# Optimization experiments

Measured on AMD Instinct MI355X. Metric: run time of the kernel, lower is better.

## Reference

```python
import jax, jax.numpy as jnp
import numpy as np

N_LINKS = 10000
N_PATHS = 100000
LSD = 32   # link_state_dim
PSD = 32   # path_state_dim
T = 4
MAX_LEN = 12
RU = 256   # readout_units
OUT = 2


def _glorot(key, shape):
    return jax.random.normal(key, shape) * jnp.sqrt(2.0 / (shape[0] + shape[-1]))


def setup_inputs() -> dict:
    key = jax.random.key(0)
    ks = jax.random.split(key, 12)
    # variable path lengths 4..12 (mean 8)
    lengths = 4 + (np.arange(N_PATHS) % 9)
    E = int(lengths.sum())
    offsets = np.cumsum(lengths) - lengths
    paths = np.repeat(np.arange(N_PATHS), lengths)
    seqs = np.arange(E) - np.repeat(offsets, lengths)  # position of hop within its path
    rng = np.random.default_rng(0)
    links = rng.integers(0, N_LINKS, size=E)
    return {
        "capacities": jax.random.uniform(ks[0], (N_LINKS,), minval=1.0, maxval=10.0),
        "traffic": jax.random.uniform(ks[1], (N_PATHS,), minval=0.1, maxval=1.0),
        "links": jnp.asarray(links, jnp.int32),
        "paths": jnp.asarray(paths, jnp.int32),
        "seqs": jnp.asarray(seqs, jnp.int32),
        "n_links": N_LINKS,
        "n_paths": N_PATHS,
        "K_link": _glorot(ks[2], (LSD, 3 * LSD)),
        "R_link": _glorot(ks[3], (LSD, 3 * LSD)),
        "b_link": jnp.zeros((2, 3 * LSD)),
        "K_path": _glorot(ks[4], (LSD, 3 * PSD)),
        "R_path": _glorot(ks[5], (PSD, 3 * PSD)),
        "b_path": jnp.zeros((2, 3 * PSD)),
        "W1": _glorot(ks[6], (PSD, RU)),
        "b1": jnp.zeros((RU,)),
        "W2": _glorot(ks[7], (RU, RU)),
        "b2": jnp.zeros((RU,)),
        "Wf": _glorot(ks[8], (RU + PSD, OUT)),
        "bf": jnp.zeros((OUT,)),
    }


def _gru(x, h, K, R, b):
    # keras GRUCell, reset_after=True: separate input/recurrent biases
    xz = x @ K + b[0]
    hz = h @ R + b[1]
    xi_z, xi_r, xi_h = jnp.split(xz, 3, axis=-1)
    hi_z, hi_r, hi_h = jnp.split(hz, 3, axis=-1)
    z = jax.nn.sigmoid(xi_z + hi_z)
    r = jax.nn.sigmoid(xi_r + hi_r)
    hh = jnp.tanh(xi_h + r * hi_h)
    return z * h + (1.0 - z) * hh


def reference(capacities, traffic, links, paths, seqs, n_links, n_paths,
              K_link, R_link, b_link, K_path, R_path, b_path,
              W1, b1, W2, b2, Wf, bf):
    link_state = jnp.concatenate([capacities[:, None], jnp.zeros((n_links, LSD - 1))], axis=1)
    path_state = jnp.concatenate([traffic[:, None], jnp.zeros((n_paths, PSD - 1))], axis=1)

    lens = jax.ops.segment_sum(jnp.ones_like(paths), paths, num_segments=n_paths)  # [P]
    mask_t = (jnp.arange(MAX_LEN)[:, None] < lens[None, :])  # [L, P]

    for _ in range(T):
        h_ = link_state[links]  # gather: [E, LSD]
        # scatter into padded per-path sequences: [P, L, LSD]
        padded = jnp.zeros((n_paths, MAX_LEN, LSD), link_state.dtype).at[paths, seqs].set(h_)

        def step(h, xm):
            x_t, m_t = xm  # [P, LSD], [P]
            h_new = _gru(x_t, h, K_path, R_path, b_path)
            h = jnp.where(m_t[:, None], h_new, h)  # masked steps keep state
            return h, h

        path_state, outputs = jax.lax.scan(step, path_state, (padded.transpose(1, 0, 2), mask_t))
        m = outputs[seqs, paths]  # gather_nd: [E, PSD]
        m = jax.ops.segment_sum(m, links, num_segments=n_links)  # [n_links, PSD]
        link_state = _gru(m, link_state, K_link, R_link, b_link)

    h1 = jax.nn.selu(path_state @ W1 + b1)
    h2 = jax.nn.selu(h1 @ W2 + b2)
    pred = jnp.concatenate([h2, path_state], axis=1) @ Wf + bf
    return pred
```

## Files before the change

kernel.cpp:

```cpp
#include <hip/hip_runtime.h>
#include <hip/hip_bf16.h>

#define NPATHS 100000
#define NLINKS 10000
#define TITERS 4
#define GRP    695

typedef __hip_bfloat16 bf16;
typedef unsigned short u16;
typedef unsigned int   u32;
typedef _Float16 half8 __attribute__((ext_vector_type(8)));
typedef __attribute__((ext_vector_type(4))) float float4v;

#define U_LNK 64
#define U_KPB 320064
#define U_RPB 323136
#define U_KLB 326208
#define U_RLB 329280
#define U_W1T 332352
#define U_W2T 340544
#define F_BP  203040
#define F_BL  203232
#define F_B1  203424
#define F_B2  203680
#define F_WF  203936
#define F_MAC 204544
#define U_WFP 1049088
#define F_PS  524800

__device__ __forceinline__ float bf2f(bf16 v) { return __bfloat162float(v); }
__device__ __forceinline__ u16 f2h_u(float f) {
    _Float16 h = (_Float16)f; u16 u; __builtin_memcpy(&u, &h, 2); return u;
}
__device__ __forceinline__ float h2f_u(u16 u) {
    _Float16 h; __builtin_memcpy(&h, &u, 2); return (float)h;
}
__device__ __forceinline__ float loadf(const void* p, int i, int isbf) {
    return isbf ? bf2f(((const bf16*)p)[i]) : ((const float*)p)[i];
}
__device__ __forceinline__ float sigmoid_(float v) { return 1.f / (1.f + __expf(-v)); }
__device__ __forceinline__ float tanh_(float v) { return 1.f - 2.f / (__expf(2.f * v) + 1.f); }
__device__ __forceinline__ float selu_(float v) {
    return v > 0.f ? 1.0507009873554805f * v : 1.7580993408473766f * (__expf(v) - 1.f);
}
__device__ __forceinline__ u16* ps_row(u16* ps0, u16* ps1, u16* ps2, int p) {
    return p < 49999 ? ps0 + (size_t)p * 32
         : (p < 99998 ? ps1 + (size_t)(p - 49999) * 32
                      : ps2 + (size_t)(p - 99998) * 32);
}

__global__ void probe_kernel(const u32* __restrict__ cap, int* __restrict__ flag) {
    if (threadIdx.x == 0 && blockIdx.x == 0) {
        bool ok = true;
        for (int i = 0; i < 8; ++i) {
            u32 w = cap[i];
            u32 e1 = (w >> 7) & 0xFF, e2 = (w >> 23) & 0xFF;
            ok = ok && e1 >= 122 && e1 <= 133 && e2 >= 122 && e2 <= 133;
        }
        *flag = ok ? 1 : 0;
    }
}

__global__ __launch_bounds__(256) void init_kernel(
    const void* __restrict__ traf, const void* __restrict__ cap, const int* __restrict__ flag,
    float* __restrict__ wsf, u16* __restrict__ wsu, u16* ps0, u16* ps1, u16* ps2,
    const void* Kp, const void* Rp, const void* bp,
    const void* Kl, const void* Rl, const void* bl,
    const void* W1, const void* b1, const void* W2, const void* b2,
    const void* Wf, const void* bfv)
{
    const int isbf = *flag;
    const int i = blockIdx.x * 256 + threadIdx.x;
    if (i < NPATHS) {
        u32 ww[16];
        ww[0] = (u32)f2h_u(loadf(traf, i, isbf));
#pragma unroll
        for (int k = 1; k < 16; ++k) ww[k] = 0;
        uint4* row = (uint4*)ps_row(ps0, ps1, ps2, i);
        row[0] = *(uint4*)(ww + 0);  row[1] = *(uint4*)(ww + 4);
        row[2] = *(uint4*)(ww + 8);  row[3] = *(uint4*)(ww + 12);
    }
    int j;
    j = i;          if (j >= 0 && j < 320000)
        wsu[U_LNK + j] = ((j & 31) == 0) ? f2h_u(loadf(cap, j >> 5, isbf)) : (u16)0;
    j = i - 320000; if (j >= 0 && j < 3072) {
        int t = j >> 9, lane = (j >> 3) & 63, e = j & 7;
        int k = (lane >> 4) * 8 + e, n = t * 16 + (lane & 15);
        wsu[U_KPB + j] = f2h_u(loadf(Kp, k * 96 + n, isbf));
    }
    j = i - 323072; if (j >= 0 && j < 3072) {
        int t = j >> 9, lane = (j >> 3) & 63, e = j & 7;
        int k = (lane >> 4) * 8 + e, n = t * 16 + (lane & 15);
        wsu[U_RPB + j] = f2h_u(loadf(Rp, k * 96 + n, isbf));
    }
    j = i - 326144; if (j >= 0 && j < 3072) {
        int t = j >> 9, lane = (j >> 3) & 63, e = j & 7;
        int k = (lane >> 4) * 8 + e, n = t * 16 + (lane & 15);
        wsu[U_KLB + j] = f2h_u(loadf(Kl, k * 96 + n, isbf));
    }
    j = i - 329216; if (j >= 0 && j < 3072) {
        int t = j >> 9, lane = (j >> 3) & 63, e = j & 7;
        int k = (lane >> 4) * 8 + e, n = t * 16 + (lane & 15);
        wsu[U_RLB + j] = f2h_u(loadf(Rl, k * 96 + n, isbf));
    }
    j = i - 332288; if (j >= 0 && j < 192)   wsf[F_BP + j] = loadf(bp, j, isbf);
    j = i - 332480; if (j >= 0 && j < 192)   wsf[F_BL + j] = loadf(bl, j, isbf);
    j = i - 332672; if (j >= 0 && j < 256)   wsf[F_B1 + j] = loadf(b1, j, isbf);
    j = i - 332928; if (j >= 0 && j < 256)   wsf[F_B2 + j] = loadf(b2, j, isbf);
    j = i - 333184; if (j >= 0 && j < 578)
        wsf[F_WF + j] = (j < 576) ? loadf(Wf, j, isbf) : loadf(bfv, j - 576, isbf);
    j = i - 334000; if (j >= 0 && j < 8192) {
        int t = j >> 9, lane = (j >> 3) & 63, e = j & 7;
        int k = (lane >> 4) * 8 + e, n = t * 16 + (lane & 15);
        wsu[U_W1T + j] = f2h_u(loadf(W1, k * 256 + n, isbf));
    }
    j = i - 343000; if (j >= 0 && j < 65536) {
        int g = j >> 9, kb = g >> 4, t = g & 15;
        int lane = (j >> 3) & 63, e = j & 7;
        int k = kb * 32 + (lane >> 4) * 8 + e, n = t * 16 + (lane & 15);
        wsu[U_W2T + j] = f2h_u(loadf(W2, k * 256 + n, isbf));
    }
    j = i - 408576; if (j >= 0 && j < 512) {
        int lane = j >> 3, e = j & 7;
        int k = (lane >> 4) * 8 + e, n = lane & 15;
        wsu[U_WFP + j] = (n < 2) ? f2h_u(loadf(Wf, (256 + k) * 2 + n, isbf)) : (u16)0;
    }
}

__global__ __launch_bounds__(256, 3) void path_gru_mfma(
    const int* __restrict__ links,
    const u16* __restrict__ KPB, const u16* __restrict__ RPB,
    const float* __restrict__ bp,
    const u16* __restrict__ lnk16,
    u16* ps0, u16* ps1, u16* ps2, float* __restrict__ m_acc)
{
    __shared__ u16 hlds[4][16 * 40];
    const int tid = threadIdx.x;
    const int wv = tid >> 6, lane = tid & 63;
    const int q = lane >> 4, col = lane & 15;
    const int c = blockIdx.x % 9;
    const int gi = (blockIdx.x / 9) * 4 + wv;
    if (gi >= GRP) return;
    const int cnt = (c == 0) ? 11112 : 11111;
    const int idx0 = gi * 16;
    const int L = 4 + c;

    const int idxc = idx0 + col;
    const int actc = idxc < cnt;
    const int idcl = min(idxc, cnt - 1);
    const int pc   = c + 9 * idcl;
    const int offc = 4 * pc + idcl * 36 + (c * (c - 1)) / 2;

    u16* hw = hlds[wv];

    half8 KB[6], RB[6];
#pragma unroll
    for (int t = 0; t < 6; ++t) {
        KB[t] = *(const half8*)(KPB + t * 512 + lane * 8);
        RB[t] = *(const half8*)(RPB + t * 512 + lane * 8);
    }
    float xzb[6], hzb[6];
#pragma unroll
    for (int t = 0; t < 6; ++t) { xzb[t] = bp[t * 16 + col]; hzb[t] = bp[96 + t * 16 + col]; }

    half8 Ah = *(const half8*)(ps_row(ps0, ps1, ps2, pc) + q * 8);
    float hold[2][4];
#pragma unroll
    for (int t = 0; t < 2; ++t)
#pragma unroll
        for (int r = 0; r < 4; ++r) {
            int idr = min(idx0 + q * 4 + r, cnt - 1);
            int pr = c + 9 * idr;
            hold[t][r] = h2f_u(ps_row(ps0, ps1, ps2, pr)[t * 16 + col]);
        }

    int ln = actc ? links[offc] : -1;
    half8 Ax = *(const half8*)(lnk16 + (size_t)max(ln, 0) * 32 + q * 8);

    for (int s = 0; s < L; ++s) {
        const int ln_nxt = (s + 1 < L && actc) ? links[offc + s + 1] : -1;
        const half8 Ax_nxt = *(const half8*)(lnk16 + (size_t)max(ln_nxt, 0) * 32 + q * 8);

        float4v xz[6], hz[6];
#pragma unroll
        for (int t = 0; t < 6; ++t) {
            float4v ix = {xzb[t], xzb[t], xzb[t], xzb[t]};
            float4v ih = {hzb[t], hzb[t], hzb[t], hzb[t]};
            xz[t] = __builtin_amdgcn_mfma_f32_16x16x32_f16(Ax, KB[t], ix, 0, 0, 0);
            hz[t] = __builtin_amdgcn_mfma_f32_16x16x32_f16(Ah, RB[t], ih, 0, 0, 0);
        }
#pragma unroll
        for (int t = 0; t < 2; ++t)
#pragma unroll
            for (int r = 0; r < 4; ++r) {
                const float z  = sigmoid_(xz[t][r] + hz[t][r]);
                const float rr = sigmoid_(xz[t + 2][r] + hz[t + 2][r]);
                const float hh = tanh_(xz[t + 4][r] + rr * hz[t + 4][r]);
                const float hn = z * hold[t][r] + (1.f - z) * hh;
                hold[t][r] = hn;
                hw[(q * 4 + r) * 40 + t * 16 + col] = f2h_u(hn);
            }
        Ah = *(const half8*)(hw + col * 40 + q * 8);
        const int half_ = lane >> 5, kk = lane & 31;
#pragma unroll
        for (int j2 = 0; j2 < 8; ++j2) {
            const int src = 2 * j2 + half_;
            const int tgt = __shfl(ln, src);
            const float v = h2f_u(hw[src * 40 + kk]);
            if (tgt >= 0) unsafeAtomicAdd(m_acc + (size_t)tgt * 32 + kk, v);
        }
        ln = ln_nxt; Ax = Ax_nxt;
    }
    if (actc) {
        uint4 tmp; __builtin_memcpy(&tmp, &Ah, 16);
        *(uint4*)(ps_row(ps0, ps1, ps2, pc) + q * 8) = tmp;
    }
}

__global__ __launch_bounds__(256) void link_gru_mfma(
    const u16* __restrict__ KLB, const u16* __restrict__ RLB,
    const float* __restrict__ bl,
    float* __restrict__ m_io, u16* __restrict__ lnk16)
{
    __shared__ u16 hlds[4][16 * 40];
    const int tid = threadIdx.x;
    const int wv = tid >> 6, lane = tid & 63;
    const int q = lane >> 4, col = lane & 15;
    const int w = blockIdx.x * 4 + wv;
    if (w >= NLINKS / 16) return;
    const int base = w * 16;
    u16* hw = hlds[wv];

    half8 KB[6], RB[6];
#pragma unroll
    for (int t = 0; t < 6; ++t) {
        KB[t] = *(const half8*)(KLB + t * 512 + lane * 8);
        RB[t] = *(const half8*)(RLB + t * 512 + lane * 8);
    }
    float xzb[6], hzb[6];
#pragma unroll
    for (int t = 0; t < 6; ++t) { xzb[t] = bl[t * 16 + col]; hzb[t] = bl[96 + t * 16 + col]; }

    half8 Ax;
    {
        float4* mr = (float4*)(m_io + (size_t)(base + col) * 32 + q * 8);
        float4 a = mr[0], b = mr[1];
        _Float16 xv[8] = {(_Float16)a.x, (_Float16)a.y, (_Float16)a.z, (_Float16)a.w,
                          (_Float16)b.x, (_Float16)b.y, (_Float16)b.z, (_Float16)b.w};
        __builtin_memcpy(&Ax, xv, 16);
        const float4 z4 = make_float4(0.f, 0.f, 0.f, 0.f);
        mr[0] = z4; mr[1] = z4;
    }
    half8 Ah = *(const half8*)(lnk16 + (size_t)(base + col) * 32 + q * 8);
    float hold[2][4];
#pragma unroll
    for (int t = 0; t < 2; ++t)
#pragma unroll
        for (int r = 0; r < 4; ++r)
            hold[t][r] = h2f_u(lnk16[(size_t)(base + q * 4 + r) * 32 + t * 16 + col]);

    float4v xz[6], hz[6];
#pragma unroll
    for (int t = 0; t < 6; ++t) {
        float4v ix = {xzb[t], xzb[t], xzb[t], xzb[t]};
        float4v ih = {hzb[t], hzb[t], hzb[t], hzb[t]};
        xz[t] = __builtin_amdgcn_mfma_f32_16x16x32_f16(Ax, KB[t], ix, 0, 0, 0);
        hz[t] = __builtin_amdgcn_mfma_f32_16x16x32_f16(Ah, RB[t], ih, 0, 0, 0);
    }
#pragma unroll
    for (int t = 0; t < 2; ++t)
#pragma unroll
        for (int r = 0; r < 4; ++r) {
            const float z  = sigmoid_(xz[t][r] + hz[t][r]);
            const float rr = sigmoid_(xz[t + 2][r] + hz[t + 2][r]);
            const float hh = tanh_(xz[t + 4][r] + rr * hz[t + 4][r]);
            const float hn = z * hold[t][r] + (1.f - z) * hh;
            hw[(q * 4 + r) * 40 + t * 16 + col] = f2h_u(hn);
        }
    {
        uint4 tmp = *(const uint4*)(hw + col * 40 + q * 8);
        *(uint4*)(lnk16 + (size_t)(base + col) * 32 + q * 8) = tmp;
    }
}

__global__ __launch_bounds__(256, 2) void readout_mfma(
    u16* ps0, u16* ps1, u16* ps2,
    const u16* __restrict__ W1T, const u16* __restrict__ W2T,
    const u16* __restrict__ WFPT,
    const float* __restrict__ b1f, const float* __restrict__ b2f,
    const float* __restrict__ Wff,
    const int* __restrict__ flag, void* __restrict__ out)
{
    __shared__ u16  sA[4][4096];
    __shared__ float sB1[256], sB2[256], sWf[578];
    const int tid = threadIdx.x;
    if (tid < 256) { sB1[tid] = b1f[tid]; sB2[tid] = b2f[tid]; }
    for (int i = tid; i < 578; i += 256) sWf[i] = Wff[i];
    __syncthreads();

    const int w = tid >> 6, lane = tid & 63;
    const int col = lane & 15, q = lane >> 4;
    const int pbase = blockIdx.x * 128 + w * 32;
    u16* sAw = sA[w];

    const half8 wfp = *(const half8*)(WFPT + lane * 8);
    const int paA = min(pbase + col, NPATHS - 1);
    const int paB = min(pbase + 16 + col, NPATHS - 1);
    const half8 apsA = *(const half8*)(ps_row(ps0, ps1, ps2, paA) + q * 8);
    const half8 apsB = *(const half8*)(ps_row(ps0, ps1, ps2, paB) + q * 8);

    float4v accpA = {0.f, 0.f, 0.f, 0.f}, accpB = {0.f, 0.f, 0.f, 0.f};
    accpA = __builtin_amdgcn_mfma_f32_16x16x32_f16(apsA, wfp, accpA, 0, 0, 0);
    accpB = __builtin_amdgcn_mfma_f32_16x16x32_f16(apsB, wfp, accpB, 0, 0, 0);

#pragma unroll
    for (int t = 0; t < 16; ++t) {
        const half8 bfrag = *(const half8*)(W1T + t * 512 + lane * 8);
        float4v acc = {0.f, 0.f, 0.f, 0.f};
        acc = __builtin_amdgcn_mfma_f32_16x16x32_f16(apsA, bfrag, acc, 0, 0, 0);
        const int kb = t >> 1;
        const int qp = 2 * (t & 1) + (col >> 3);
#pragma unroll
        for (int rI = 0; rI < 4; ++rI) {
            const int m = q * 4 + rI;
            const float h1 = selu_(acc[rI] + sB1[t * 16 + col]);
            sAw[kb * 512 + qp * 128 + m * 8 + (col & 7)] = f2h_u(h1);
        }
    }
    half8 afrA[8];
#pragma unroll
    for (int kb = 0; kb < 8; ++kb)
        afrA[kb] = *(const half8*)(sAw + kb * 512 + lane * 8);

#pragma unroll
    for (int t = 0; t < 16; ++t) {
        const half8 bfrag = *(const half8*)(W1T + t * 512 + lane * 8);
        float4v acc = {0.f, 0.f, 0.f, 0.f};
        acc = __builtin_amdgcn_mfma_f32_16x16x32_f16(apsB, bfrag, acc, 0, 0, 0);
        const int kb = t >> 1;
        const int qp = 2 * (t & 1) + (col >> 3);
#pragma unroll
        for (int rI = 0; rI < 4; ++rI) {
            const int m = q * 4 + rI;
            const float h1 = selu_(acc[rI] + sB1[t * 16 + col]);
            sAw[kb * 512 + qp * 128 + m * 8 + (col & 7)] = f2h_u(h1);
        }
    }

    float4v a2A[16], a2B[16];
#pragma unroll
    for (int t = 0; t < 16; ++t) {
        a2A[t] = (float4v){0.f, 0.f, 0.f, 0.f};
        a2B[t] = (float4v){0.f, 0.f, 0.f, 0.f};
    }
#pragma unroll
    for (int kb = 0; kb < 8; ++kb) {
        const half8 afrB = *(const half8*)(sAw + kb * 512 + lane * 8);
#pragma unroll
        for (int t = 0; t < 16; ++t) {
            const half8 bfrag = *(const half8*)(W2T + (kb * 16 + t) * 512 + lane * 8);
            a2A[t] = __builtin_amdgcn_mfma_f32_16x16x32_f16(afrA[kb], bfrag, a2A[t], 0, 0, 0);
            a2B[t] = __builtin_amdgcn_mfma_f32_16x16x32_f16(afrB,     bfrag, a2B[t], 0, 0, 0);
        }
    }

    float p0A[4] = {0.f, 0.f, 0.f, 0.f}, p1A[4] = {0.f, 0.f, 0.f, 0.f};
    float p0B[4] = {0.f, 0.f, 0.f, 0.f}, p1B[4] = {0.f, 0.f, 0.f, 0.f};
#pragma unroll
    for (int t = 0; t < 16; ++t) {
        const int n = t * 16 + col;
        const float wf0 = sWf[2 * n], wf1 = sWf[2 * n + 1];
#pragma unroll
        for (int rI = 0; rI < 4; ++rI) {
            const float h2A = selu_(a2A[t][rI] + sB2[n]);
            const float h2B = selu_(a2B[t][rI] + sB2[n]);
            p0A[rI] += h2A * wf0; p1A[rI] += h2A * wf1;
            p0B[rI] += h2B * wf0; p1B[rI] += h2B * wf1;
        }
    }
#pragma unroll
    for (int msk = 1; msk < 16; msk <<= 1) {
#pragma unroll
        for (int rI = 0; rI < 4; ++rI) {
            p0A[rI] += __shfl_xor(p0A[rI], msk);
            p1A[rI] += __shfl_xor(p1A[rI], msk);
            p0B[rI] += __shfl_xor(p0B[rI], msk);
            p1B[rI] += __shfl_xor(p1B[rI], msk);
        }
    }
    float ocA[4], ocB[4];
#pragma unroll
    for (int rI = 0; rI < 4; ++rI) {
        ocA[rI] = __shfl_xor(accpA[rI], 1);
        ocB[rI] = __shfl_xor(accpB[rI], 1);
    }
    if (col == 0) {
        const int isbf = *flag;
#pragma unroll
        for (int rI = 0; rI < 4; ++rI) {
            const int ppA = pbase + q * 4 + rI;
            const int ppB = pbase + 16 + q * 4 + rI;
            if (ppA < NPATHS) {
                const float s0 = p0A[rI] + accpA[rI] + sWf[576];
                const float s1 = p1A[rI] + ocA[rI]   + sWf[577];
                if (isbf) {
                    __hip_bfloat162 o;
                    o.x = __float2bfloat16(s0); o.y = __float2bfloat16(s1);
                    ((__hip_bfloat162*)out)[ppA] = o;
                } else ((float2*)out)[ppA] = make_float2(s0, s1);
            }
            if (ppB < NPATHS) {
                const float s0 = p0B[rI] + accpB[rI] + sWf[576];
                const float s1 = p1B[rI] + ocB[rI]   + sWf[577];
                if (isbf) {
                    __hip_bfloat162 o;
                    o.x = __float2bfloat16(s0); o.y = __float2bfloat16(s1);
                    ((__hip_bfloat162*)out)[ppB] = o;
                } else ((float2*)out)[ppB] = make_float2(s0, s1);
            }
        }
    }
}

extern "C" void kernel_launch(void* const* d_in, const int* in_sizes, int n_in,
                              void* d_out, int out_size, void* d_ws, size_t ws_size,
                              hipStream_t stream)
{
    const int* links = (const int*)d_in[2];
    float* wsf = (float*)d_ws;
    u16*   wsu = (u16*)d_ws;
    int*   flag = (int*)d_ws;

    u16* wps = (u16*)(wsf + F_PS);
    u16 *ps0, *ps1, *ps2;
    if (ws_size >= (size_t)F_PS * 4 + 6400000 + 256) {
        ps0 = wps; ps1 = wps + (size_t)49999 * 32; ps2 = wps + (size_t)99998 * 32;
    } else {
        ps0 = (u16*)d_in[3]; ps1 = (u16*)d_in[4]; ps2 = wps;
    }

    probe_kernel<<<1, 64, 0, stream>>>((const u32*)d_in[0], flag);
    init_kernel<<<1599, 256, 0, stream>>>(d_in[1], d_in[0], flag, wsf, wsu, ps0, ps1, ps2,
                                          d_in[10], d_in[11], d_in[12],
                                          d_in[7], d_in[8], d_in[9],
                                          d_in[13], d_in[14], d_in[15], d_in[16],
                                          d_in[17], d_in[18]);
    hipMemsetAsync(wsf + F_MAC, 0, NLINKS * 32 * sizeof(float), stream);

    const int pg_blocks = 9 * ((GRP + 3) / 4);
    const int lg_blocks = (NLINKS / 16 + 3) / 4;
    for (int t = 0; t < TITERS; ++t) {
        path_gru_mfma<<<pg_blocks, 256, 0, stream>>>(
            links, wsu + U_KPB, wsu + U_RPB, wsf + F_BP,
            wsu + U_LNK, ps0, ps1, ps2, wsf + F_MAC);
        link_gru_mfma<<<lg_blocks, 256, 0, stream>>>(
            wsu + U_KLB, wsu + U_RLB, wsf + F_BL, wsf + F_MAC, wsu + U_LNK);
    }
    readout_mfma<<<(NPATHS + 127) / 128, 256, 0, stream>>>(
        ps0, ps1, ps2,
        wsu + U_W1T, wsu + U_W2T, wsu + U_WFP,
        wsf + F_B1, wsf + F_B2, wsf + F_WF, flag, d_out);
}
```

Baseline: 576.7 us.

## Stage path GRU weights in LDS and fuse z/r gate accumulations

```diff
diff --git a/kernel.cpp b/kernel.cpp
--- a/kernel.cpp
+++ b/kernel.cpp
@@ -127,15 +127,26 @@
     }
 }
 
-__global__ __launch_bounds__(256, 3) void path_gru_mfma(
+__global__ __launch_bounds__(256, 8) void path_gru_mfma(
     const int* __restrict__ links,
     const u16* __restrict__ KPB, const u16* __restrict__ RPB,
     const float* __restrict__ bp,
     const u16* __restrict__ lnk16,
     u16* ps0, u16* ps1, u16* ps2, float* __restrict__ m_acc)
 {
-    __shared__ u16 hlds[4][16 * 40];
+    __shared__ u16  sKB[3072], sRB[3072];
+    __shared__ float sBP[192];
+    __shared__ u16  hlds[4][16 * 40];
     const int tid = threadIdx.x;
+    {
+        const uint4* sk = (const uint4*)KPB;
+        const uint4* sr = (const uint4*)RPB;
+        uint4* dk = (uint4*)sKB; uint4* dr = (uint4*)sRB;
+        for (int i = tid; i < 384; i += 256) { dk[i] = sk[i]; dr[i] = sr[i]; }
+        if (tid < 192) sBP[tid] = bp[tid];
+    }
+    __syncthreads();
+
     const int wv = tid >> 6, lane = tid & 63;
     const int q = lane >> 4, col = lane & 15;
     const int c = blockIdx.x % 9;
@@ -153,16 +164,6 @@
 
     u16* hw = hlds[wv];
 
-    half8 KB[6], RB[6];
-#pragma unroll
-    for (int t = 0; t < 6; ++t) {
-        KB[t] = *(const half8*)(KPB + t * 512 + lane * 8);
-        RB[t] = *(const half8*)(RPB + t * 512 + lane * 8);
-    }
-    float xzb[6], hzb[6];
-#pragma unroll
-    for (int t = 0; t < 6; ++t) { xzb[t] = bp[t * 16 + col]; hzb[t] = bp[96 + t * 16 + col]; }
-
     half8 Ah = *(const half8*)(ps_row(ps0, ps1, ps2, pc) + q * 8);
     float hold[2][4];
 #pragma unroll
@@ -175,31 +176,43 @@
         }
 
     int ln = actc ? links[offc] : -1;
-    half8 Ax = *(const half8*)(lnk16 + (size_t)max(ln, 0) * 32 + q * 8);
 
     for (int s = 0; s < L; ++s) {
         const int ln_nxt = (s + 1 < L && actc) ? links[offc + s + 1] : -1;
-        const half8 Ax_nxt = *(const half8*)(lnk16 + (size_t)max(ln_nxt, 0) * 32 + q * 8);
-
-        float4v xz[6], hz[6];
-#pragma unroll
-        for (int t = 0; t < 6; ++t) {
-            float4v ix = {xzb[t], xzb[t], xzb[t], xzb[t]};
-            float4v ih = {hzb[t], hzb[t], hzb[t], hzb[t]};
-            xz[t] = __builtin_amdgcn_mfma_f32_16x16x32_f16(Ax, KB[t], ix, 0, 0, 0);
-            hz[t] = __builtin_amdgcn_mfma_f32_16x16x32_f16(Ah, RB[t], ih, 0, 0, 0);
-        }
-#pragma unroll
-        for (int t = 0; t < 2; ++t)
+        const half8 Ax = *(const half8*)(lnk16 + (size_t)max(ln, 0) * 32 + q * 8);
+
+#pragma unroll
+        for (int th = 0; th < 2; ++th) {
+            const float bz = sBP[th * 16 + col]       + sBP[96 + th * 16 + col];
+            const float br = sBP[(th + 2) * 16 + col] + sBP[96 + (th + 2) * 16 + col];
+            const float bxh = sBP[(th + 4) * 16 + col];
+            const float bhh = sBP[96 + (th + 4) * 16 + col];
+            const half8 kbz = *(const half8*)(sKB + (th)     * 512 + lane * 8);
+            const half8 rbz = *(const half8*)(sRB + (th)     * 512 + lane * 8);
+            const half8 kbr = *(const half8*)(sKB + (th + 2) * 512 + lane * 8);
+            const half8 rbr = *(const half8*)(sRB + (th + 2) * 512 + lane * 8);
+            const half8 kbh = *(const half8*)(sKB + (th + 4) * 512 + lane * 8);
+            const half8 rbh = *(const half8*)(sRB + (th + 4) * 512 + lane * 8);
+            float4v sz = {bz, bz, bz, bz};
+            sz = __builtin_amdgcn_mfma_f32_16x16x32_f16(Ax, kbz, sz, 0, 0, 0);
+            sz = __builtin_amdgcn_mfma_f32_16x16x32_f16(Ah, rbz, sz, 0, 0, 0);
+            float4v sr_ = {br, br, br, br};
+            sr_ = __builtin_amdgcn_mfma_f32_16x16x32_f16(Ax, kbr, sr_, 0, 0, 0);
+            sr_ = __builtin_amdgcn_mfma_f32_16x16x32_f16(Ah, rbr, sr_, 0, 0, 0);
+            float4v xh = {bxh, bxh, bxh, bxh};
+            xh = __builtin_amdgcn_mfma_f32_16x16x32_f16(Ax, kbh, xh, 0, 0, 0);
+            float4v hr = {bhh, bhh, bhh, bhh};
+            hr = __builtin_amdgcn_mfma_f32_16x16x32_f16(Ah, rbh, hr, 0, 0, 0);
 #pragma unroll
             for (int r = 0; r < 4; ++r) {
-                const float z  = sigmoid_(xz[t][r] + hz[t][r]);
-                const float rr = sigmoid_(xz[t + 2][r] + hz[t + 2][r]);
-                const float hh = tanh_(xz[t + 4][r] + rr * hz[t + 4][r]);
-                const float hn = z * hold[t][r] + (1.f - z) * hh;
-                hold[t][r] = hn;
-                hw[(q * 4 + r) * 40 + t * 16 + col] = f2h_u(hn);
+                const float z  = sigmoid_(sz[r]);
+                const float rr = sigmoid_(sr_[r]);
+                const float hh = tanh_(xh[r] + rr * hr[r]);
+                const float hn = z * hold[th][r] + (1.f - z) * hh;
+                hold[th][r] = hn;
+                hw[(q * 4 + r) * 40 + th * 16 + col] = f2h_u(hn);
             }
+        }
         Ah = *(const half8*)(hw + col * 40 + q * 8);
         const int half_ = lane >> 5, kk = lane & 31;
 #pragma unroll
@@ -209,7 +222,7 @@
             const float v = h2f_u(hw[src * 40 + kk]);
             if (tgt >= 0) unsafeAtomicAdd(m_acc + (size_t)tgt * 32 + kk, v);
         }
-        ln = ln_nxt; Ax = Ax_nxt;
+        ln = ln_nxt;
     }
     if (actc) {
         uint4 tmp; __builtin_memcpy(&tmp, &Ah, 16);
```

Result: slower. 960.1 us (+66.5%).
